# Kernel tuning notes

Hardware: AMD Instinct MI355X
Metric: run time of the kernel (lower is better)

The kernel has to match this reference:

```python
import jax, jax.numpy as jnp
import numpy as np

DIM = 256
HEADS = 4
WIN = 128
PAD = (WIN - 1) // 2  # 63
SHIFT = WIN // 2      # 64
RED = 16              # SE reduction


def _hann(w):
    # torch.hann_window(w, periodic=False)
    n = jnp.arange(w, dtype=jnp.float32)
    return 0.5 * (1.0 - jnp.cos(2.0 * jnp.pi * n / (w - 1)))


def _layernorm(x, g, b, eps=1e-5):
    mu = jnp.mean(x, axis=-1, keepdims=True)
    var = jnp.var(x, axis=-1, keepdims=True)
    return (x - mu) * jax.lax.rsqrt(var + eps) * g + b


def _attend_windows(x, ln_g, ln_b, in_proj_w, in_proj_b, out_w, out_b):
    B, T, C = x.shape
    w = WIN
    h = HEADS
    d = C // h
    L = T + 2 * PAD - w + 1  # number of stride-1 windows (= T-1 for even w)
    y = _layernorm(x, ln_g, ln_b)
    y_pad = jnp.pad(y, ((0, 0), (PAD, PAD), (0, 0)))
    idx = jnp.arange(L)[:, None] + jnp.arange(w)[None, :]  # (L, w)
    win = y_pad[:, idx, :]  # (B, L, w, C) -- the unfold blowup
    win = win * _hann(w)[None, None, :, None]
    # fused qkv projection (torch MHA in_proj)
    qkv = jnp.einsum('blwc,ec->blwe', win, in_proj_w) + in_proj_b  # (B,L,w,3C)
    q, k, v = jnp.split(qkv, 3, axis=-1)
    q = q.reshape(B, L, w, h, d)
    k = k.reshape(B, L, w, h, d)
    v = v.reshape(B, L, w, h, d)
    scale = 1.0 / jnp.sqrt(jnp.asarray(d, dtype=x.dtype))
    scores = jnp.einsum('blqhd,blkhd->blhqk', q, k) * scale
    attn = jax.nn.softmax(scores, axis=-1)
    o = jnp.einsum('blhqk,blkhd->blqhd', attn, v).reshape(B, L, w, C)
    o = jnp.einsum('blwc,ec->blwe', o, out_w) + out_b  # out_proj
    # fold: overlap-add back to length T (crop padding)
    idx_flat = idx.reshape(-1)  # (L*w,)
    acc = jnp.zeros((B, T + 2 * PAD, C), dtype=x.dtype)
    acc = acc.at[:, idx_flat, :].add(o.reshape(B, L * w, C))
    y_out = acc[:, PAD:PAD + T, :]
    counts = jnp.zeros((T + 2 * PAD,), dtype=x.dtype).at[idx_flat].add(1.0)
    counts = counts[PAD:PAD + T]
    return y_out / (counts[None, :, None] + 1e-6)


def setup_inputs() -> dict:
    key = jax.random.key(0)
    ks = jax.random.split(key, 9)
    C = DIM
    s = 0.02
    return {
        'x': jax.random.normal(ks[0], (1, 1024, C), dtype=jnp.float32),
        'ln_g': jnp.ones((C,), jnp.float32),
        'ln_b': jnp.zeros((C,), jnp.float32),
        'in_proj_w': jax.random.normal(ks[1], (3 * C, C), jnp.float32) * s,
        'in_proj_b': jnp.zeros((3 * C,), jnp.float32),
        'out_w': jax.random.normal(ks[2], (C, C), jnp.float32) * s,
        'out_b': jnp.zeros((C,), jnp.float32),
        'proj_w': jax.random.normal(ks[3], (C, C), jnp.float32) * s,
        'proj_b': jnp.zeros((C,), jnp.float32),
        'se_w1': jax.random.normal(ks[4], (C // RED, C), jnp.float32) * s,
        'se_w2': jax.random.normal(ks[5], (C, C // RED), jnp.float32) * s,
    }


def reference(x, ln_g, ln_b, in_proj_w, in_proj_b, out_w, out_b, proj_w, proj_b, se_w1, se_w2):
    # T > window_size branch (1024 > 128)
    y_main = _attend_windows(x, ln_g, ln_b, in_proj_w, in_proj_b, out_w, out_b)
    x_shift = jnp.roll(x, SHIFT, axis=1)
    y_shift = _attend_windows(x_shift, ln_g, ln_b, in_proj_w, in_proj_b, out_w, out_b)
    y_shift = jnp.roll(y_shift, -SHIFT, axis=1)
    y = 0.5 * (y_main + y_shift)
    y = jnp.einsum('btc,ec->bte', y, proj_w) + proj_b  # proj (dropout p=0 -> identity)
    # SE module: global average over T, bottleneck MLP, sigmoid gate
    s = jnp.mean(y, axis=1)  # (B, C)
    s = jax.nn.relu(s @ se_w1.T)
    s = jax.nn.sigmoid(s @ se_w2.T)
    y = y * s[:, None, :]
    return x + y
```

## Files before the change

### kernel.cpp

```cpp
#include <hip/hip_runtime.h>

#define TLEN 1024
#define CDIM 256
#define NHEAD 4
#define HD 64
#define WIN_ 128
#define PADL 63
#define LWIN 1023
#define TPAD 1150
#define SW 32

typedef __attribute__((ext_vector_type(8))) short bf16x8;
typedef __attribute__((ext_vector_type(8))) _Float16 f16x8;
typedef __attribute__((ext_vector_type(2))) __fp16 fp16v2;
typedef __attribute__((ext_vector_type(4))) float f32x4;

__device__ __forceinline__ int prow(int v, int t) {
  if (v == 0) return t;
  if (t < PADL || t >= PADL + TLEN) return t;
  int s = t - PADL;
  s = (s + (TLEN - 64)) & (TLEN - 1);
  return PADL + s;
}

__device__ __forceinline__ float hannf(int j) {
  return 0.5f * (1.0f - __cosf(6.283185307179586f * (float)j / 127.0f));
}

__device__ __forceinline__ float countf(int t) {
  int lo = t - 127; if (lo < 0) lo = 0;
  int hi = t;       if (hi > LWIN - 1) hi = LWIN - 1;
  return (float)(hi - lo + 1);
}

__device__ __forceinline__ unsigned short bfr(float f) {
  unsigned int u = __float_as_uint(f);
  u += 0x7FFFu + ((u >> 16) & 1u);
  return (unsigned short)(u >> 16);
}
__device__ __forceinline__ unsigned int pk2t(float a, float b) {
  return __builtin_amdgcn_perm(__float_as_uint(b), __float_as_uint(a), 0x07060302u);
}
__device__ __forceinline__ float bfu(unsigned short u) {
  return __uint_as_float(((unsigned int)u) << 16);
}
__device__ __forceinline__ float bflo(unsigned int u) { return __uint_as_float(u << 16); }
__device__ __forceinline__ float bfhi(unsigned int u) { return __uint_as_float(u & 0xFFFF0000u); }

__device__ __forceinline__ float ex2(float x) {
  float r;
  asm("v_exp_f32 %0, %1" : "=v"(r) : "v"(x));
  return r;
}
__device__ __forceinline__ float rcpf(float x) {
  float r;
  asm("v_rcp_f32 %0, %1" : "=v"(r) : "v"(x));
  return r;
}

__device__ __forceinline__ unsigned int pkh(float lo, float hi) {
  union { fp16v2 h; unsigned int u; } c;
  c.h = __builtin_amdgcn_cvt_pkrtz(lo, hi);
  return c.u;
}
__device__ __forceinline__ unsigned short h16(float f) {
  union { _Float16 h; unsigned short u; } c;
  c.h = (_Float16)f;
  return c.u;
}
__device__ __forceinline__ unsigned int pkmul(unsigned int a, unsigned int b) {
  unsigned int r;
  asm("v_pk_mul_f16 %0, %1, %2" : "=v"(r) : "v"(a), "v"(b));
  return r;
}
__device__ __forceinline__ unsigned int exp2pk(unsigned int x) {
  unsigned int lo, hi;
  unsigned int xh = x >> 16;
  asm("v_exp_f16 %0, %1" : "=v"(lo) : "v"(x));
  asm("v_exp_f16 %0, %1" : "=v"(hi) : "v"(xh));
  return __builtin_amdgcn_perm(hi, lo, 0x05040100u);
}

#define AL16(h, l) ((((unsigned int)(l)) >> 16) | (((unsigned int)(h)) << 16))

#define QLOG2E 0.18033688011112042f

__global__ void k_prep(const float* __restrict__ x, const float* __restrict__ g,
                       const float* __restrict__ b, unsigned short* __restrict__ lnbf,
                       const float* __restrict__ W, unsigned short* __restrict__ Wb,
                       const float* __restrict__ pw, const float* __restrict__ ow,
                       const float* __restrict__ ob, unsigned short* __restrict__ Mtb,
                       float* __restrict__ vbv,
                       float* __restrict__ accg, unsigned short* __restrict__ Pbf,
                       float* __restrict__ msum) {
  __shared__ float pr[256];
  __shared__ float red[4];
  const int bid = blockIdx.x;
  const int tid = threadIdx.x;
  if (bid < 256) {
    int wv = tid >> 6, lane = tid & 63;
    int r = bid * 4 + wv;
    float4 v = ((const float4*)(x + (size_t)r * CDIM))[lane];
    float s = v.x + v.y + v.z + v.w;
    float q = v.x * v.x + v.y * v.y + v.z * v.z + v.w * v.w;
    #pragma unroll
    for (int m = 32; m >= 1; m >>= 1) { s += __shfl_xor(s, m); q += __shfl_xor(q, m); }
    float mu = s * (1.0f / 256.0f);
    float var = q * (1.0f / 256.0f) - mu * mu;
    float rs = rsqrtf(var + 1e-5f);
    float4 gg = ((const float4*)g)[lane];
    float4 bb = ((const float4*)b)[lane];
    uint2 o;
    o.x = (unsigned int)bfr((v.x - mu) * rs * gg.x + bb.x) |
          ((unsigned int)bfr((v.y - mu) * rs * gg.y + bb.y) << 16);
    o.y = (unsigned int)bfr((v.z - mu) * rs * gg.z + bb.z) |
          ((unsigned int)bfr((v.w - mu) * rs * gg.w + bb.w) << 16);
    ((uint2*)(lnbf + (size_t)r * CDIM))[lane] = o;
  } else if (bid < 352) {
    int i = (bid - 256) * 256 + tid;
    const float4* src = (const float4*)W;
    float4 a = src[2 * i], c = src[2 * i + 1];
    uint4 o;
    o.x = (unsigned int)bfr(a.x) | ((unsigned int)bfr(a.y) << 16);
    o.y = (unsigned int)bfr(a.z) | ((unsigned int)bfr(a.w) << 16);
    o.z = (unsigned int)bfr(c.x) | ((unsigned int)bfr(c.y) << 16);
    o.w = (unsigned int)bfr(c.z) | ((unsigned int)bfr(c.w) << 16);
    ((uint4*)Wb)[i] = o;
  } else if (bid < 608) {
    const int e = bid - 352;
    pr[tid] = pw[(size_t)e * CDIM + tid];
    __syncthreads();
    float a0 = 0.f, a1 = 0.f, a2 = 0.f, a3 = 0.f;
    for (int m = 0; m < 256; m += 4) {
      a0 += pr[m] * ow[(size_t)m * CDIM + tid];
      a1 += pr[m + 1] * ow[(size_t)(m + 1) * CDIM + tid];
      a2 += pr[m + 2] * ow[(size_t)(m + 2) * CDIM + tid];
      a3 += pr[m + 3] * ow[(size_t)(m + 3) * CDIM + tid];
    }
    Mtb[(size_t)e * CDIM + tid] = bfr((a0 + a1) + (a2 + a3));
    float rv = pr[tid] * ob[tid];
    #pragma unroll
    for (int m = 32; m >= 1; m >>= 1) rv += __shfl_xor(rv, m);
    if ((tid & 63) == 0) red[tid >> 6] = rv;
    __syncthreads();
    if (tid == 0) vbv[e] = (red[0] + red[1]) + (red[2] + red[3]);
  } else if (bid < 736) {
    uint4 zz = make_uint4(0, 0, 0, 0);
    for (int i = (bid - 608) * 256 + tid; i < 147200; i += 128 * 256)
      ((uint4*)accg)[i] = zz;
  } else {
    uint4 zz = make_uint4(0, 0, 0, 0);
    for (int i = (bid - 736) * 256 + tid; i < 12096; i += 32 * 256) {
      int idx = (i < 6048) ? i : (104352 + (i - 6048));
      ((uint4*)Pbf)[idx] = zz;
    }
    if (bid == 767 && tid < 64) ((float4*)msum)[tid] = make_float4(0.f, 0.f, 0.f, 0.f);
  }
}

__launch_bounds__(512, 1)
__global__ void k_proj(const unsigned short* __restrict__ lnbf,
                       const unsigned short* __restrict__ Wb,
                       unsigned short* __restrict__ Pbf) {
  __shared__ __align__(16) unsigned short Ps[32 * 128];
  const int tid = threadIdx.x;
  const int lane = tid & 63, wv = tid >> 6;
  const int li16 = lane & 15, q4 = lane >> 4;
  const int ws = wv & 1, we = wv >> 1;
  const int sbase = blockIdx.x * 32;
  const int ebase = blockIdx.y * 128;
  const int s0 = sbase + ws * 16;
  const int e0 = ebase + we * 32;

  f32x4 acc[2];
  acc[0] = (f32x4){0.f, 0.f, 0.f, 0.f};
  acc[1] = (f32x4){0.f, 0.f, 0.f, 0.f};

  #pragma unroll
  for (int ks = 0; ks < 8; ++ks) {
    bf16x8 Af = *(const bf16x8*)(lnbf + (size_t)(s0 + li16) * 256 + ks * 32 + q4 * 8);
    #pragma unroll
    for (int et = 0; et < 2; ++et) {
      bf16x8 Bf = *(const bf16x8*)(Wb + (size_t)(e0 + 16 * et + li16) * 256 + ks * 32 + q4 * 8);
      acc[et] = __builtin_amdgcn_mfma_f32_16x16x32_bf16(Af, Bf, acc[et], 0, 0, 0);
    }
  }
  #pragma unroll
  for (int et = 0; et < 2; ++et)
    #pragma unroll
    for (int r = 0; r < 4; ++r) {
      int lr = ws * 16 + 4 * q4 + r;
      int lc = we * 32 + 16 * et + li16;
      Ps[lr * 128 + lc] = bfr(acc[et][r]);
    }
  __syncthreads();
  {
    int r = tid >> 4, c = (tid & 15) * 8;
    *(uint4*)(Pbf + (size_t)(PADL + sbase + r) * 768 + ebase + c) = *(uint4*)&Ps[r * 128 + c];
  }
}

__device__ __forceinline__ void stage_load(const unsigned short* __restrict__ Pbf,
                                           int v, int hd, int l0, int w, int stid,
                                           uint4& A, uint4& B) {
  const int jp = stid & 63;
  const int dg = stid >> 6;
  const int j0 = 2 * jp;
  int row0 = prow(v, l0 + w + j0);
  int row1 = prow(v, l0 + w + j0 + 1);
  A = *(const uint4*)(Pbf + (size_t)row0 * 768 + 512 + hd * 64 + dg * 8);
  B = *(const uint4*)(Pbf + (size_t)row1 * 768 + 512 + hd * 64 + dg * 8);
}

__device__ __forceinline__ void stage_write(unsigned short* vt, int w, int stid,
                                            const float* __restrict__ bB,
                                            const float* __restrict__ hth,
                                            uint4 a, uint4 b) {
  const int jp = stid & 63;
  const int dg = stid >> 6;
  const int j0 = 2 * jp;
  const int p0 = w + j0;
  float h0 = hth[j0], h1 = hth[j0 + 1];
  float e0 = ex2(h0 * bB[p0]);
  float e1 = ex2(h1 * bB[p0 + 1]);
  float f0 = e0 * h0, f1 = e1 * h1;
  unsigned int av[4] = {a.x, a.y, a.z, a.w};
  unsigned int bv[4] = {b.x, b.y, b.z, b.w};
  #pragma unroll
  for (int q = 0; q < 4; ++q) {
    int d0 = dg * 8 + 2 * q;
    unsigned int w0 = pkh(f0 * bflo(av[q]), f1 * bflo(bv[q]));
    unsigned int w1 = pkh(f0 * bfhi(av[q]), f1 * bfhi(bv[q]));
    *(unsigned int*)&vt[d0 * 128 + (j0 ^ ((d0 & 7) << 3))] = w0;
    *(unsigned int*)&vt[(d0 + 1) * 128 + (j0 ^ (((d0 + 1) & 7) << 3))] = w1;
  }
  if (stid < 64) {
    *(unsigned int*)&vt[64 * 128 + j0] = pkh(e0, e1);
  }
}

__launch_bounds__(1024, 4)
__global__ void k_attn(const unsigned short* __restrict__ Pbf, const float* __restrict__ ipb,
                       float* __restrict__ accg) {
  __shared__ __align__(16) unsigned short band[160 * 168];
  __shared__ __align__(16) unsigned short Vt[2][80 * 128];
  __shared__ __align__(16) unsigned char uni[159 * 68 * 4];
  __shared__ float hth[128];
  __shared__ float bB[160];
  __shared__ float bqS[64];

  unsigned short* Pq = (unsigned short*)uni;
  unsigned short* Pk = Pq + 159 * 64;
  float* accs = (float*)uni;

  const int strip = blockIdx.x, hd = blockIdx.y, v = blockIdx.z;
  const int l0 = strip * SW;
  const int nw = (SW < LWIN - l0) ? SW : (LWIN - l0);
  const int span = nw - 1 + WIN_;
  const int tid = threadIdx.x;
  const int lane = tid & 63;
  const int wv16 = tid >> 6;
  const int wg = wv16 >> 3;
  const int wv = wv16 & 7;
  const int stid = tid & 511;
  const int li16 = lane & 15, q4 = lane >> 4;
  const int iw = 16 * wv + li16;

  uint4 sA, sB;
  stage_load(Pbf, v, hd, l0, wg, stid, sA, sB);

  if (tid < 128) hth[tid] = hannf(tid);
  if (tid < 64) bqS[tid] = ipb[hd * 64 + tid];
  for (int i = tid; i < span * 8; i += 1024) {
    int t = i >> 3, dg = i & 7;
    int row = prow(v, l0 + t);
    const unsigned short* src = Pbf + (size_t)row * 768 + hd * 64;
    uint4 q = *(const uint4*)(src + dg * 8);
    uint4 k = *(const uint4*)(src + 256 + dg * 8);
    int off = (dg * 8) ^ ((t & 7) << 3);
    *(uint4*)&Pq[t * 64 + off] = q;
    *(uint4*)&Pk[t * 64 + off] = k;
  }
  {
    uint4 zz = make_uint4(0, 0, 0, 0);
    for (int i = tid; i < 480; i += 1024) {
      int bidx = i / 240, k = i % 240;
      *(uint4*)&Vt[bidx][65 * 128 + k * 8] = zz;
    }
  }
  __syncthreads();

  for (int p = tid; p < span; p += 1024) {
    float b = 0.0f;
    int sw = (p & 7) << 3;
    for (int d = 0; d < 64; ++d) b += bqS[d] * bfu(Pk[p * 64 + (d ^ sw)]);
    bB[p] = b * QLOG2E;
  }
  for (int tile = wv16; tile < 100; tile += 16) {
    int ta = tile / 10, tb = tile - 10 * (tile / 10);
    int tqa = 16 * ta + li16, swq = (tqa & 7) << 3;
    bf16x8 Aq0 = *(bf16x8*)&Pq[tqa * 64 + ((8 * q4) ^ swq)];
    bf16x8 Aq1 = *(bf16x8*)&Pq[tqa * 64 + ((32 + 8 * q4) ^ swq)];
    int tkb = 16 * tb + li16, swk = (tkb & 7) << 3;
    bf16x8 Bk0 = *(bf16x8*)&Pk[tkb * 64 + ((8 * q4) ^ swk)];
    bf16x8 Bk1 = *(bf16x8*)&Pk[tkb * 64 + ((32 + 8 * q4) ^ swk)];
    f32x4 D = (f32x4){0.f, 0.f, 0.f, 0.f};
    D = __builtin_amdgcn_mfma_f32_16x16x32_bf16(Aq0, Bk0, D, 0, 0, 0);
    D = __builtin_amdgcn_mfma_f32_16x16x32_bf16(Aq1, Bk1, D, 0, 0, 0);
    #pragma unroll
    for (int r = 0; r < 4; ++r)
      band[(16 * ta + 4 * q4 + r) * 168 + 16 * tb + li16] = h16(D[r]);
  }
  __syncthreads();

  for (int i = tid; i < 159 * 68; i += 1024) accs[i] = 0.0f;
  if (wg == 0) stage_write(&Vt[0][0], 0, stid, bB, hth, sA, sB);
  else         stage_write(&Vt[1][0], 1, stid, bB, hth, sA, sB);
  __syncthreads();

  unsigned int hh2p[16];
  {
    const float h_i = hth[iw];
    #pragma unroll
    for (int ks = 0; ks < 4; ++ks)
      #pragma unroll
      for (int q = 0; q < 4; ++q) {
        float lo = h_i * hth[32 * ks + 8 * q4 + 2 * q] * QLOG2E;
        float hi = h_i * hth[32 * ks + 8 * q4 + 2 * q + 1] * QLOG2E;
        hh2p[ks * 4 + q] = pkh(lo, hi);
      }
  }

  #pragma unroll 1
  for (int wp = 0; wp < nw; wp += 2) {
    const int w = wp + wg;
    const bool act = (w < nw);
    const int wnext = wp + 2 + wg;
    if (wnext < nw) stage_load(Pbf, v, hd, l0, wnext, stid, sA, sB);

    f32x4 O[5];
    #pragma unroll
    for (int mt = 0; mt < 5; ++mt) O[mt] = (f32x4){0.f, 0.f, 0.f, 0.f};

    if (act) {
      const int m = w & 7;
      const unsigned short* brow = &band[(w + iw) * 168 + (w & ~7)];
      const unsigned short* vt = &Vt[wg][0];

      #pragma unroll
      for (int ks = 0; ks < 4; ++ks) {
        uint4 R0 = *(const uint4*)&brow[32 * ks + 8 * q4];
        uint4 R1 = *(const uint4*)&brow[32 * ks + 8 * q4 + 8];
        unsigned int d0 = R0.x, d1 = R0.y, d2 = R0.z, d3 = R0.w;
        unsigned int d4 = R1.x, d5 = R1.y, d6 = R1.z, d7 = R1.w;
        unsigned int o0, o1, o2, o3;
        switch (m) {
          case 0: o0 = d0; o1 = d1; o2 = d2; o3 = d3; break;
          case 1: o0 = AL16(d1, d0); o1 = AL16(d2, d1); o2 = AL16(d3, d2); o3 = AL16(d4, d3); break;
          case 2: o0 = d1; o1 = d2; o2 = d3; o3 = d4; break;
          case 3: o0 = AL16(d2, d1); o1 = AL16(d3, d2); o2 = AL16(d4, d3); o3 = AL16(d5, d4); break;
          case 4: o0 = d2; o1 = d3; o2 = d4; o3 = d5; break;
          case 5: o0 = AL16(d3, d2); o1 = AL16(d4, d3); o2 = AL16(d5, d4); o3 = AL16(d6, d5); break;
          case 6: o0 = d3; o1 = d4; o2 = d5; o3 = d6; break;
          default: o0 = AL16(d4, d3); o1 = AL16(d5, d4); o2 = AL16(d6, d5); o3 = AL16(d7, d6); break;
        }
        unsigned int m0 = pkmul(hh2p[ks * 4 + 0], o0);
        unsigned int m1 = pkmul(hh2p[ks * 4 + 1], o1);
        unsigned int m2 = pkmul(hh2p[ks * 4 + 2], o2);
        unsigned int m3 = pkmul(hh2p[ks * 4 + 3], o3);
        union { uint4 u; f16x8 f; } cvt;
        cvt.u.x = exp2pk(m0);
        cvt.u.y = exp2pk(m1);
        cvt.u.z = exp2pk(m2);
        cvt.u.w = exp2pk(m3);
        f16x8 Bf = cvt.f;

        __builtin_amdgcn_s_setprio(1);
        #pragma unroll
        for (int mt = 0; mt < 5; ++mt) {
          int d = 16 * mt + li16;
          f16x8 Af = *(const f16x8*)&vt[d * 128 + ((32 * ks + 8 * q4) ^ ((d & 7) << 3))];
          O[mt] = __builtin_amdgcn_mfma_f32_16x16x32_f16(Af, Bf, O[mt], 0, 0, 0);
        }
        __builtin_amdgcn_s_setprio(0);
      }
    }

    if (wg == 0) {
      float nn = __shfl(O[4][0], li16);
      float sc = rcpf(nn);
      float* arow = &accs[(w + iw) * 68];
      #pragma unroll
      for (int mt = 0; mt < 4; ++mt) {
        int c = 16 * mt + 4 * q4;
        float4 cur = *(float4*)&arow[c];
        cur.x += O[mt][0] * sc; cur.y += O[mt][1] * sc;
        cur.z += O[mt][2] * sc; cur.w += O[mt][3] * sc;
        *(float4*)&arow[c] = cur;
      }
    }
    __syncthreads();

    if (wg == 1 && act) {
      float nn = __shfl(O[4][0], li16);
      float sc = rcpf(nn);
      float* arow = &accs[(w + iw) * 68];
      #pragma unroll
      for (int mt = 0; mt < 4; ++mt) {
        int c = 16 * mt + 4 * q4;
        float4 cur = *(float4*)&arow[c];
        cur.x += O[mt][0] * sc; cur.y += O[mt][1] * sc;
        cur.z += O[mt][2] * sc; cur.w += O[mt][3] * sc;
        *(float4*)&arow[c] = cur;
      }
    }
    if (wnext < nw) stage_write(&Vt[wg][0], wnext, stid, bB, hth, sA, sB);
    __syncthreads();
  }

  float* av = accg + (size_t)v * TPAD * CDIM;
  for (int i = tid; i < span * 64; i += 1024) {
    int p = i >> 6, dd = i & 63;
    int lo = p - 127; if (lo < 0) lo = 0;
    int hi = p; if (hi > nw - 1) hi = nw - 1;
    float cnt = (float)(hi - lo + 1);
    float bvd = ipb[512 + hd * 64 + dd];
    atomicAdd(&av[(size_t)(l0 + p) * CDIM + hd * 64 + dd],
              accs[p * 68 + dd] + cnt * bvd);
  }
}

__launch_bounds__(512, 2)
__global__ void k_comb(const float* __restrict__ accg, const unsigned short* __restrict__ Mtb,
                       const float* __restrict__ vbv, const float* __restrict__ pb,
                       float* __restrict__ z, float* __restrict__ msum) {
  __shared__ __align__(16) unsigned short Ub[32 * 264];
  __shared__ float cfA[32], cfB[32], bscL[32];
  __shared__ float msB[128];
  const int tid = threadIdx.x;
  const int lane = tid & 63, wv = tid >> 6;
  const int li16 = lane & 15, q4 = lane >> 4;
  const int t0 = blockIdx.x * 32;
  const int e0 = blockIdx.y * 128;

  if (tid < 32) {
    int s = t0 + tid;
    float c0 = countf(PADL + s);
    float c1 = countf(PADL + ((s + 64) & (TLEN - 1)));
    float fA = 0.5f / (c0 + 1e-6f), fB = 0.5f / (c1 + 1e-6f);
    cfA[tid] = fA; cfB[tid] = fB;
    bscL[tid] = c0 * fA + c1 * fB;
  }
  if (tid < 128) msB[tid] = 0.0f;
  __syncthreads();

  for (int i = tid; i < 32 * 128; i += 512) {
    int rr = i >> 7, c2 = (i & 127) * 2;
    int s = t0 + rr;
    int s1 = (s + 64) & (TLEN - 1);
    float2 a0 = *(const float2*)&accg[(size_t)(PADL + s) * CDIM + c2];
    float2 a1 = *(const float2*)&accg[(size_t)TPAD * CDIM + (size_t)(PADL + s1) * CDIM + c2];
    float fA = cfA[rr], fB = cfB[rr];
    *(unsigned int*)&Ub[rr * 264 + c2] =
        pk2t(a0.x * fA + a1.x * fB, a0.y * fA + a1.y * fB);
  }
  __syncthreads();

  f32x4 acc[2];
  acc[0] = (f32x4){0.f, 0.f, 0.f, 0.f};
  acc[1] = (f32x4){0.f, 0.f, 0.f, 0.f};
  #pragma unroll
  for (int ks = 0; ks < 8; ++ks) {
    bf16x8 Bf = *(const bf16x8*)(Mtb + (size_t)(e0 + wv * 16 + li16) * 256 + ks * 32 + q4 * 8);
    #pragma unroll
    for (int it = 0; it < 2; ++it) {
      bf16x8 Af = *(bf16x8*)&Ub[(16 * it + li16) * 264 + ks * 32 + q4 * 8];
      acc[it] = __builtin_amdgcn_mfma_f32_16x16x32_bf16(Af, Bf, acc[it], 0, 0, 0);
    }
  }

  {
    int e = e0 + wv * 16 + li16;
    float vbe = vbv[e], pbe = pb[e];
    float part = 0.0f;
    #pragma unroll
    for (int it = 0; it < 2; ++it)
      #pragma unroll
      for (int r = 0; r < 4; ++r) {
        int rloc = 16 * it + 4 * q4 + r;
        float val = acc[it][r] + bscL[rloc] * vbe + pbe;
        z[(size_t)(t0 + rloc) * CDIM + e] = val;
        part += val;
      }
    atomicAdd(&msB[e - e0], part);
  }
  __syncthreads();
  if (tid < 128) atomicAdd(&msum[e0 + tid], msB[tid]);
}

__global__ void k_finalse(const float* __restrict__ x, const float* __restrict__ z,
                          const float* __restrict__ msum, const float* __restrict__ w1,
                          const float* __restrict__ w2, float* __restrict__ out) {
  __shared__ float red2[16][4];
  __shared__ float s1[16];
  __shared__ float gateS[256];
  int tid = threadIdx.x;
  int lane = tid & 63, wv = tid >> 6;
  float sm = msum[tid] * (1.0f / 1024.0f);
  #pragma unroll
  for (int r = 0; r < 16; ++r) {
    float v = sm * w1[(size_t)r * 256 + tid];
    #pragma unroll
    for (int m = 32; m >= 1; m >>= 1) v += __shfl_xor(v, m);
    if (lane == 0) red2[r][wv] = v;
  }
  __syncthreads();
  if (tid < 16) {
    float a = red2[tid][0] + red2[tid][1] + red2[tid][2] + red2[tid][3];
    s1[tid] = fmaxf(a, 0.0f);
  }
  __syncthreads();
  float gacc = 0.0f;
  #pragma unroll
  for (int i = 0; i < 16; ++i) gacc += s1[i] * w2[(size_t)tid * 16 + i];
  gateS[tid] = 1.0f / (1.0f + __expf(-gacc));
  __syncthreads();
  int i = blockIdx.x * 256 + tid;
  float4 xv = ((const float4*)x)[i];
  float4 zv = ((const float4*)z)[i];
  float4 gv = ((const float4*)gateS)[i & 63];
  float4 o;
  o.x = xv.x + zv.x * gv.x;
  o.y = xv.y + zv.y * gv.y;
  o.z = xv.z + zv.z * gv.z;
  o.w = xv.w + zv.w * gv.w;
  ((float4*)out)[i] = o;
}

extern "C" void kernel_launch(void* const* d_in, const int* in_sizes, int n_in,
                              void* d_out, int out_size, void* d_ws, size_t ws_size,
                              hipStream_t stream) {
  const float* x   = (const float*)d_in[0];
  const float* lng = (const float*)d_in[1];
  const float* lnb = (const float*)d_in[2];
  const float* ipw = (const float*)d_in[3];
  const float* ipb = (const float*)d_in[4];
  const float* ow  = (const float*)d_in[5];
  const float* ob  = (const float*)d_in[6];
  const float* pw  = (const float*)d_in[7];
  const float* pb  = (const float*)d_in[8];
  const float* w1  = (const float*)d_in[9];
  const float* w2  = (const float*)d_in[10];
  float* out = (float*)d_out;

  float* ws = (float*)d_ws;
  unsigned short* lnbf = (unsigned short*)ws;
  unsigned short* Wb   = (unsigned short*)(ws + 131072);
  unsigned short* Pbf  = (unsigned short*)(ws + 229376);
  float* accg = ws + 229376 + 441600;
  unsigned short* Mtb = (unsigned short*)(accg + 588800);
  float* vbv  = accg + 588800 + 32768;
  float* z    = vbv + 256;
  float* msum = z + 262144;

  k_prep<<<dim3(768), dim3(256), 0, stream>>>(x, lng, lnb, lnbf, ipw, Wb,
                                              pw, ow, ob, Mtb, vbv, accg, Pbf, msum);
  k_proj<<<dim3(32, 6), dim3(512), 0, stream>>>(lnbf, Wb, Pbf);
  k_attn<<<dim3(32, NHEAD, 2), dim3(1024), 0, stream>>>(Pbf, ipb, accg);
  k_comb<<<dim3(32, 2), dim3(512), 0, stream>>>(accg, Mtb, vbv, pb, z, msum);
  k_finalse<<<dim3(256), dim3(256), 0, stream>>>(x, z, msum, w1, w2, out);
}
```

Measured before the change: 170.8 us.

## Fuse combine and SE-gate kernels via cooperative grid sync

Merges the combine GEMM kernel and the SE/final residual kernel into one cooperative kernel that does a grid-wide sync after accumulating the channel sums. The grid is reshaped to 128 blocks of 16 rows each, so each block does a single MFMA tile and later writes its own slice of the output. This removes one kernel launch and the gap between launches. In exchange it adds a grid barrier, and every block redundantly recomputes the tiny SE MLP.

```diff
diff --git a/kernel.cpp b/kernel.cpp
--- a/kernel.cpp
+++ b/kernel.cpp
@@ -1,4 +1,5 @@
 #include <hip/hip_runtime.h>
+#include <hip/hip_cooperative_groups.h>
 
 #define TLEN 1024
 #define CDIM 256
@@ -431,19 +432,24 @@
 }
 
 __launch_bounds__(512, 2)
-__global__ void k_comb(const float* __restrict__ accg, const unsigned short* __restrict__ Mtb,
-                       const float* __restrict__ vbv, const float* __restrict__ pb,
-                       float* __restrict__ z, float* __restrict__ msum) {
-  __shared__ __align__(16) unsigned short Ub[32 * 264];
-  __shared__ float cfA[32], cfB[32], bscL[32];
+__global__ void k_combfin(const float* __restrict__ accg, const unsigned short* __restrict__ Mtb,
+                          const float* __restrict__ vbv, const float* __restrict__ pb,
+                          float* __restrict__ z, float* __restrict__ msum,
+                          const float* __restrict__ x, const float* __restrict__ w1,
+                          const float* __restrict__ w2, float* __restrict__ out) {
+  __shared__ __align__(16) unsigned short Ub[16 * 264];
+  __shared__ float cfA[16], cfB[16], bscL[16];
   __shared__ float msB[128];
+  __shared__ float red2[16][4];
+  __shared__ float s1g[16];
+  __shared__ float gateS[256];
   const int tid = threadIdx.x;
   const int lane = tid & 63, wv = tid >> 6;
   const int li16 = lane & 15, q4 = lane >> 4;
-  const int t0 = blockIdx.x * 32;
-  const int e0 = blockIdx.y * 128;
-
-  if (tid < 32) {
+  const int t0 = (blockIdx.x >> 1) * 16;
+  const int e0 = (blockIdx.x & 1) * 128;
+
+  if (tid < 16) {
     int s = t0 + tid;
     float c0 = countf(PADL + s);
     float c1 = countf(PADL + ((s + 64) & (TLEN - 1)));
@@ -454,7 +460,7 @@
   if (tid < 128) msB[tid] = 0.0f;
   __syncthreads();
 
-  for (int i = tid; i < 32 * 128; i += 512) {
+  for (int i = tid; i < 16 * 128; i += 512) {
     int rr = i >> 7, c2 = (i & 127) * 2;
     int s = t0 + rr;
     int s1 = (s + 64) & (TLEN - 1);
@@ -466,17 +472,12 @@
   }
   __syncthreads();
 
-  f32x4 acc[2];
-  acc[0] = (f32x4){0.f, 0.f, 0.f, 0.f};
-  acc[1] = (f32x4){0.f, 0.f, 0.f, 0.f};
+  f32x4 acc = (f32x4){0.f, 0.f, 0.f, 0.f};
   #pragma unroll
   for (int ks = 0; ks < 8; ++ks) {
     bf16x8 Bf = *(const bf16x8*)(Mtb + (size_t)(e0 + wv * 16 + li16) * 256 + ks * 32 + q4 * 8);
-    #pragma unroll
-    for (int it = 0; it < 2; ++it) {
-      bf16x8 Af = *(bf16x8*)&Ub[(16 * it + li16) * 264 + ks * 32 + q4 * 8];
-      acc[it] = __builtin_amdgcn_mfma_f32_16x16x32_bf16(Af, Bf, acc[it], 0, 0, 0);
-    }
+    bf16x8 Af = *(bf16x8*)&Ub[li16 * 264 + ks * 32 + q4 * 8];
+    acc = __builtin_amdgcn_mfma_f32_16x16x32_bf16(Af, Bf, acc, 0, 0, 0);
   }
 
   {
@@ -484,57 +485,52 @@
     float vbe = vbv[e], pbe = pb[e];
     float part = 0.0f;
     #pragma unroll
-    for (int it = 0; it < 2; ++it)
-      #pragma unroll
-      for (int r = 0; r < 4; ++r) {
-        int rloc = 16 * it + 4 * q4 + r;
-        float val = acc[it][r] + bscL[rloc] * vbe + pbe;
-        z[(size_t)(t0 + rloc) * CDIM + e] = val;
-        part += val;
-      }
+    for (int r = 0; r < 4; ++r) {
+      int rloc = 4 * q4 + r;
+      float val = acc[r] + bscL[rloc] * vbe + pbe;
+      z[(size_t)(t0 + rloc) * CDIM + e] = val;
+      part += val;
+    }
     atomicAdd(&msB[e - e0], part);
   }
   __syncthreads();
   if (tid < 128) atomicAdd(&msum[e0 + tid], msB[tid]);
-}
-
-__global__ void k_finalse(const float* __restrict__ x, const float* __restrict__ z,
-                          const float* __restrict__ msum, const float* __restrict__ w1,
-                          const float* __restrict__ w2, float* __restrict__ out) {
-  __shared__ float red2[16][4];
-  __shared__ float s1[16];
-  __shared__ float gateS[256];
-  int tid = threadIdx.x;
-  int lane = tid & 63, wv = tid >> 6;
-  float sm = msum[tid] * (1.0f / 1024.0f);
+
+  cooperative_groups::this_grid().sync();
+
+  float sm = (tid < 256) ? msum[tid] * (1.0f / 1024.0f) : 0.0f;
   #pragma unroll
   for (int r = 0; r < 16; ++r) {
-    float v = sm * w1[(size_t)r * 256 + tid];
+    float v = (tid < 256) ? sm * w1[(size_t)r * 256 + tid] : 0.0f;
     #pragma unroll
     for (int m = 32; m >= 1; m >>= 1) v += __shfl_xor(v, m);
-    if (lane == 0) red2[r][wv] = v;
+    if (lane == 0 && wv < 4) red2[r][wv] = v;
   }
   __syncthreads();
   if (tid < 16) {
     float a = red2[tid][0] + red2[tid][1] + red2[tid][2] + red2[tid][3];
-    s1[tid] = fmaxf(a, 0.0f);
-  }
-  __syncthreads();
-  float gacc = 0.0f;
-  #pragma unroll
-  for (int i = 0; i < 16; ++i) gacc += s1[i] * w2[(size_t)tid * 16 + i];
-  gateS[tid] = 1.0f / (1.0f + __expf(-gacc));
-  __syncthreads();
-  int i = blockIdx.x * 256 + tid;
-  float4 xv = ((const float4*)x)[i];
-  float4 zv = ((const float4*)z)[i];
-  float4 gv = ((const float4*)gateS)[i & 63];
-  float4 o;
-  o.x = xv.x + zv.x * gv.x;
-  o.y = xv.y + zv.y * gv.y;
-  o.z = xv.z + zv.z * gv.z;
-  o.w = xv.w + zv.w * gv.w;
-  ((float4*)out)[i] = o;
+    s1g[tid] = fmaxf(a, 0.0f);
+  }
+  __syncthreads();
+  if (tid < 256) {
+    float gacc = 0.0f;
+    #pragma unroll
+    for (int i = 0; i < 16; ++i) gacc += s1g[i] * w2[(size_t)tid * 16 + i];
+    gateS[tid] = 1.0f / (1.0f + __expf(-gacc));
+  }
+  __syncthreads();
+  {
+    int i = blockIdx.x * 512 + tid;
+    float4 xv = ((const float4*)x)[i];
+    float4 zv = ((const float4*)z)[i];
+    float4 gv = ((const float4*)gateS)[i & 63];
+    float4 o;
+    o.x = xv.x + zv.x * gv.x;
+    o.y = xv.y + zv.y * gv.y;
+    o.z = xv.z + zv.z * gv.z;
+    o.w = xv.w + zv.w * gv.w;
+    ((float4*)out)[i] = o;
+  }
 }
 
 extern "C" void kernel_launch(void* const* d_in, const int* in_sizes, int n_in,
@@ -567,6 +563,9 @@
                                               pw, ow, ob, Mtb, vbv, accg, Pbf, msum);
   k_proj<<<dim3(32, 6), dim3(512), 0, stream>>>(lnbf, Wb, Pbf);
   k_attn<<<dim3(32, NHEAD, 2), dim3(1024), 0, stream>>>(Pbf, ipb, accg);
-  k_comb<<<dim3(32, 2), dim3(512), 0, stream>>>(accg, Mtb, vbv, pb, z, msum);
-  k_finalse<<<dim3(256), dim3(256), 0, stream>>>(x, z, msum, w1, w2, out);
-}
+  {
+    void* args[] = {(void*)&accg, (void*)&Mtb, (void*)&vbv, (void*)&pb, (void*)&z,
+                    (void*)&msum, (void*)&x, (void*)&w1, (void*)&w2, (void*)&out};
+    hipLaunchCooperativeKernel((const void*)k_combfin, dim3(128), dim3(512), args, 0, stream);
+  }
+}
```

Measured after the change: 210.3 us. 23.2% more time.
